# Kernel optimization log

Measured on AMD Instinct MI355X. Metric: run time of the kernel, lower is better.

## Reference

```python
import jax, jax.numpy as jnp
import numpy as np

B, T, H, P, F = 65536, 128, 1, 3, 3  # batch, input_length, hidden_dims, pred_var_dims, features


def setup_inputs() -> dict:
    key = jax.random.key(0)
    ks = jax.random.split(key, 8)
    return {
        "history_input": jax.random.normal(ks[0], (B, 1, T, F), dtype=jnp.float32),
        "h0": jnp.zeros((1, B, H), dtype=jnp.float32),
        "c0": jnp.zeros((1, B, H), dtype=jnp.float32),
        "target_acc": jax.random.normal(ks[1], (B, 1, F), dtype=jnp.float32),
        "W_ih": jax.random.normal(ks[2], (4 * H, F), dtype=jnp.float32) * 0.3,
        "W_hh": jax.random.normal(ks[3], (4 * H, H), dtype=jnp.float32) * 0.3,
        "b_ih": jnp.zeros((4 * H,), dtype=jnp.float32),
        "b_hh": jnp.zeros((4 * H,), dtype=jnp.float32),
        "W_mean": jax.random.normal(ks[4], (P, T * H), dtype=jnp.float32) * 0.05,
        "b_mean": jnp.zeros((P,), dtype=jnp.float32),
        "W_var": jax.random.normal(ks[5], (6, T * H), dtype=jnp.float32) * 0.05,
        "b_var": jnp.zeros((6,), dtype=jnp.float32),
    }


def _rotation_matrix(x):
    # x: [B, T, 3]; Gram-Schmidt on last three velocity vectors -> columns of R
    v1, v2, v3 = x[:, -1], x[:, -2], x[:, -3]
    b1 = v1 / jnp.linalg.norm(v1, axis=1, keepdims=True)
    a2 = v2 - jnp.sum(v2 * b1, axis=1, keepdims=True) * b1
    b2 = a2 / jnp.linalg.norm(a2, axis=1, keepdims=True)
    b3 = jnp.cross(b1, b2)
    sign = jnp.where(jnp.sum(v3 * b3, axis=1, keepdims=True) > 0, 1.0, -1.0)
    return jnp.stack([b1, b2, sign * b3], axis=-1)  # [B, 3, 3]


def _lstm(x, h0, c0, W_ih, W_hh, b_ih, b_hh):
    # x: [B, T, F]; PyTorch gate order i, f, g, o
    def step(carry, xt):
        h, c = carry
        g = xt @ W_ih.T + b_ih + h @ W_hh.T + b_hh
        i, f, gg, o = jnp.split(g, 4, axis=-1)
        c = jax.nn.sigmoid(f) * c + jax.nn.sigmoid(i) * jnp.tanh(gg)
        h = jax.nn.sigmoid(o) * jnp.tanh(c)
        return (h, c), h
    (hT, cT), outs = jax.lax.scan(step, (h0, c0), jnp.swapaxes(x, 0, 1))
    return jnp.swapaxes(outs, 0, 1), hT, cT  # [B, T, H]


def reference(history_input, h0, c0, target_acc, W_ih, W_hh, b_ih, b_hh,
              W_mean, b_mean, W_var, b_var):
    x = history_input[:, 0]                      # [B, T, 3]
    R = _rotation_matrix(x)                      # [B, 3, 3]
    rot = jnp.einsum('bji,bkj->bki', R, x)       # R^T @ x_k for each timestep

    out, hT, cT = _lstm(rot, h0[0], c0[0], W_ih, W_hh, b_ih, b_hh)
    feat = out.reshape(out.shape[0], -1)         # [B, T*H]
    means = feat @ W_mean.T + b_mean             # [B, 3]
    elements = feat @ W_var.T + b_var            # [B, 6]

    # unit-lower-triangular L (rows filled per cumsum index = [0, 1, 3])
    eye = jnp.eye(P, dtype=elements.dtype)
    lower = jnp.broadcast_to(eye, (elements.shape[0], P, P))
    lower = lower.at[:, 1, 0].set(elements[:, 0])
    lower = lower.at[:, 2, 0].set(elements[:, 1])
    lower = lower.at[:, 2, 1].set(elements[:, 2])
    dvals = jnp.exp(elements[:, 3:6])            # positive diagonal
    diag = dvals[:, None, :] * eye               # [B, 3, 3]
    sigma = lower @ diag @ jnp.swapaxes(lower, 1, 2)

    rot_target = jnp.einsum('bji,bj->bi', R, target_acc[:, 0])  # R^T @ a
    d = means - rot_target
    sigma_inv = jnp.linalg.inv(sigma)
    quad = jnp.einsum('bi,bij,bj->b', d, sigma_inv, d)
    logprob = -0.5 * dvals.sum(axis=1) - 0.5 * quad
    return -logprob.mean()
```

## Files before the change

kernel.cpp:

```cpp
#include <hip/hip_runtime.h>

#define T_STEPS 128
#define B_TOTAL 65536
#define BLOCK 256
#define REP 2
#define EPB (BLOCK / REP)
#define NBLOCKS (B_TOTAL / EPB)
#define CH 8
#define NCH (T_STEPS / CH)
#define R4S 7
#define FPT 3

#define LOG2E 1.44269504088896f

typedef __attribute__((ext_vector_type(2))) float f2;

__device__ __forceinline__ float fast_rcp(float x) {
    return __builtin_amdgcn_rcpf(x);
}
__device__ __forceinline__ float fast_exp2(float x) {
    return __builtin_amdgcn_exp2f(x);
}

__global__ __launch_bounds__(BLOCK, 2) void lstm_nll_main(
    const float* __restrict__ x,
    const float* __restrict__ h0,
    const float* __restrict__ c0,
    const float* __restrict__ target,
    const float* __restrict__ W_ih,
    const float* __restrict__ W_hh,
    const float* __restrict__ b_ih,
    const float* __restrict__ b_hh,
    const float* __restrict__ W_mean,
    const float* __restrict__ b_mean,
    const float* __restrict__ W_var,
    const float* __restrict__ b_var,
    float* __restrict__ partial)
{
    __shared__ __align__(16) float4 lds_x4[EPB * R4S];
    __shared__ float4 wpack4[T_STEPS * 3];
    __shared__ float  wavesum[BLOCK / 64];

    const int tid = threadIdx.x;

    for (int idx = tid; idx < T_STEPS * 3; idx += BLOCK) {
        const int t = idx / 3;
        const int k = idx - t * 3;
        float4 v;
        if (k == 0)      v = make_float4(W_mean[0*T_STEPS+t], W_mean[1*T_STEPS+t],
                                         W_mean[2*T_STEPS+t], W_var[0*T_STEPS+t]);
        else if (k == 1) v = make_float4(W_var[1*T_STEPS+t], W_var[2*T_STEPS+t],
                                         W_var[3*T_STEPS+t], W_var[4*T_STEPS+t]);
        else             v = make_float4(W_var[5*T_STEPS+t], 0.f, 0.f, 0.f);
        wpack4[idx] = v;
    }

    const int e = tid >> 1;
    const int b = blockIdx.x * EPB + e;
    const float* xb = x + (size_t)b * (T_STEPS * 3);

    const float hh0 = h0[b];
    const float cc0 = c0[b];
    const float t0 = target[b*3+0], t1 = target[b*3+1], t2 = target[b*3+2];

    const float v1x = xb[127*3+0], v1y = xb[127*3+1], v1z = xb[127*3+2];
    const float v2x = xb[126*3+0], v2y = xb[126*3+1], v2z = xb[126*3+2];
    const float v3x = xb[125*3+0], v3y = xb[125*3+1], v3z = xb[125*3+2];

    const float inv1 = rsqrtf(v1x*v1x + v1y*v1y + v1z*v1z);
    const float b1x = v1x*inv1, b1y = v1y*inv1, b1z = v1z*inv1;
    const float dp  = v2x*b1x + v2y*b1y + v2z*b1z;
    const float a2x = v2x - dp*b1x, a2y = v2y - dp*b1y, a2z = v2z - dp*b1z;
    const float inv2 = rsqrtf(a2x*a2x + a2y*a2y + a2z*a2z);
    const float b2x = a2x*inv2, b2y = a2y*inv2, b2z = a2z*inv2;
    float b3x = b1y*b2z - b1z*b2y;
    float b3y = b1z*b2x - b1x*b2z;
    float b3z = b1x*b2y - b1y*b2x;
    const float sgn = (v3x*b3x + v3y*b3y + v3z*b3z) > 0.0f ? 1.0f : -1.0f;
    b3x *= sgn; b3y *= sgn; b3z *= sgn;

    const float wi00 = W_ih[0], wi01 = W_ih[1],  wi02 = W_ih[2];
    const float wi10 = W_ih[3], wi11 = W_ih[4],  wi12 = W_ih[5];
    const float wi20 = W_ih[6], wi21 = W_ih[7],  wi22 = W_ih[8];
    const float wi30 = W_ih[9], wi31 = W_ih[10], wi32 = W_ih[11];
    const float s1 = -LOG2E, s2 = -2.0f * LOG2E;

    const f2 wAx = { s1*(wi00*b1x + wi01*b2x + wi02*b3x),
                     s1*(wi10*b1x + wi11*b2x + wi12*b3x) };
    const f2 wAy = { s1*(wi00*b1y + wi01*b2y + wi02*b3y),
                     s1*(wi10*b1y + wi11*b2y + wi12*b3y) };
    const f2 wAz = { s1*(wi00*b1z + wi01*b2z + wi02*b3z),
                     s1*(wi10*b1z + wi11*b2z + wi12*b3z) };
    const f2 wBx = { s2*(wi20*b1x + wi21*b2x + wi22*b3x),
                     s1*(wi30*b1x + wi31*b2x + wi32*b3x) };
    const f2 wBy = { s2*(wi20*b1y + wi21*b2y + wi22*b3y),
                     s1*(wi30*b1y + wi31*b2y + wi32*b3y) };
    const f2 wBz = { s2*(wi20*b1z + wi21*b2z + wi22*b3z),
                     s1*(wi30*b1z + wi31*b2z + wi32*b3z) };
    const f2 wAh = { s1*W_hh[0], s1*W_hh[1] };
    const f2 wBh = { s2*W_hh[2], s1*W_hh[3] };
    const f2 bgA = { s1*(b_ih[0] + b_hh[0]), s1*(b_ih[1] + b_hh[1]) };
    const f2 bgB = { s2*(b_ih[2] + b_hh[2]), s1*(b_ih[3] + b_hh[3]) };

    float h = hh0;
    float c = cc0;
    f2 P0 = {0.f, 0.f}, P1 = {0.f, 0.f}, P2 = {0.f, 0.f}, P3 = {0.f, 0.f};
    float e5a = 0.f;

    const float4* xg4 = (const float4*)(x + (size_t)blockIdx.x * EPB * (T_STEPS * 3));
    int ldsidx[FPT];
    int gidx[FPT];
    #pragma unroll
    for (int j = 0; j < FPT; ++j) {
        const int f = j * BLOCK + tid;
        const int r = f / 6;
        const int cc = f - r * 6;
        ldsidx[j] = r * R4S + cc;
        gidx[j]   = r * (T_STEPS * 3 / 4) + cc;
    }

    float4 pre[FPT];
    #pragma unroll
    for (int j = 0; j < FPT; ++j) pre[j] = xg4[gidx[j]];

    const float* rowp = (const float*)&lds_x4[e * R4S];

    for (int tc = 0; tc < NCH; ++tc) {
        __syncthreads();
        #pragma unroll
        for (int j = 0; j < FPT; ++j) {
            lds_x4[ldsidx[j]] = pre[j];
        }
        __syncthreads();

        f2 xdA[CH], xdB[CH];
        #pragma unroll
        for (int s = 0; s < CH; ++s) {
            const float xx = rowp[s*3+0], xy = rowp[s*3+1], xz = rowp[s*3+2];
            const f2 X = { xx, xx };
            const f2 Y = { xy, xy };
            const f2 Z = { xz, xz };
            xdA[s] = wAx*X + wAy*Y + wAz*Z + bgA;
            xdB[s] = wBx*X + wBy*Y + wBz*Z + bgB;
        }

        if (tc + 1 < NCH) {
            const int cb = (tc + 1) * 6;
            #pragma unroll
            for (int j = 0; j < FPT; ++j) pre[j] = xg4[gidx[j] + cb];
        }

        #pragma unroll
        for (int s = 0; s < CH; ++s) {
            const f2 H = { h, h };
            const f2 gA = wAh*H + xdA[s];
            const f2 gB = wBh*H + xdB[s];
            const float u = fast_exp2(gA.x);
            const float a = fast_exp2(gA.y);
            const float v = fast_exp2(gB.x);
            const float z = fast_exp2(gB.y);
            const float U = 1.0f + u, A = 1.0f + a, V = 1.0f + v;
            const float Q = U * V;
            const float num = __builtin_fmaf(c, Q, (2.0f - V) * A);
            const float den = Q * A;
            c = num * fast_rcp(den);
            const float wm = fminf(c * (-2.0f * LOG2E), 126.0f);
            const float w = fast_exp2(wm);
            const float W = 1.0f + w;
            h = (2.0f - W) * fast_rcp((1.0f + z) * W);
            const int t = tc * CH + s;
            const float4 w0 = wpack4[t*3 + 0];
            const float4 w1 = wpack4[t*3 + 1];
            const float4 w2 = wpack4[t*3 + 2];
            const f2 Hv = { h, h };
            P0 += ((f2){w0.x, w0.y}) * Hv;
            P1 += ((f2){w0.z, w0.w}) * Hv;
            P2 += ((f2){w1.x, w1.y}) * Hv;
            P3 += ((f2){w1.z, w1.w}) * Hv;
            e5a += w2.x * h;
        }
    }

    const float m0 = P0.x + b_mean[0];
    const float m1 = P0.y + b_mean[1];
    const float m2 = P1.x + b_mean[2];
    const float e0 = P1.y + b_var[0];
    const float e1 = P2.x + b_var[1];
    const float e2 = P2.y + b_var[2];
    const float e3 = P3.x + b_var[3];
    const float e4 = P3.y + b_var[4];
    const float e5 = e5a  + b_var[5];

    const float dv0 = fast_exp2(e3 * LOG2E);
    const float dv1 = fast_exp2(e4 * LOG2E);
    const float dv2 = fast_exp2(e5 * LOG2E);

    const float rt0 = b1x*t0 + b1y*t1 + b1z*t2;
    const float rt1 = b2x*t0 + b2y*t1 + b2z*t2;
    const float rt2 = b3x*t0 + b3y*t1 + b3z*t2;

    const float d0 = m0 - rt0, d1 = m1 - rt1, d2 = m2 - rt2;
    const float y0 = d0;
    const float y1 = d1 - e0 * y0;
    const float y2 = d2 - e1 * y0 - e2 * y1;
    const float quad = y0*y0*fast_rcp(dv0) + y1*y1*fast_rcp(dv1)
                     + y2*y2*fast_rcp(dv2);

    float contrib = 0.5f * (dv0 + dv1 + dv2) + 0.5f * quad;
    if ((tid & (REP - 1)) != 0) contrib = 0.0f;

    #pragma unroll
    for (int off = 32; off > 0; off >>= 1)
        contrib += __shfl_down(contrib, off, 64);
    const int lane = tid & 63, wid = tid >> 6;
    if (lane == 0) wavesum[wid] = contrib;
    __syncthreads();
    if (tid == 0) {
        float s = 0.f;
        #pragma unroll
        for (int w = 0; w < BLOCK / 64; ++w) s += wavesum[w];
        partial[blockIdx.x] = s;
    }
}

__global__ __launch_bounds__(256) void lstm_nll_finalize(
    const float* __restrict__ partial, float* __restrict__ out, int n)
{
    const int tid = threadIdx.x;
    float s = 0.0f;
    for (int i = tid; i < n; i += 256) s += partial[i];
    #pragma unroll
    for (int off = 32; off > 0; off >>= 1)
        s += __shfl_down(s, off, 64);
    __shared__ float wavesum[4];
    const int lane = tid & 63, wid = tid >> 6;
    if (lane == 0) wavesum[wid] = s;
    __syncthreads();
    if (tid == 0) {
        out[0] = (wavesum[0] + wavesum[1] + wavesum[2] + wavesum[3]) *
                 (1.0f / (float)B_TOTAL);
    }
}

extern "C" void kernel_launch(void* const* d_in, const int* in_sizes, int n_in,
                              void* d_out, int out_size, void* d_ws, size_t ws_size,
                              hipStream_t stream) {
    const float* x      = (const float*)d_in[0];
    const float* h0     = (const float*)d_in[1];
    const float* c0     = (const float*)d_in[2];
    const float* target = (const float*)d_in[3];
    const float* W_ih   = (const float*)d_in[4];
    const float* W_hh   = (const float*)d_in[5];
    const float* b_ih   = (const float*)d_in[6];
    const float* b_hh   = (const float*)d_in[7];
    const float* W_mean = (const float*)d_in[8];
    const float* b_mean = (const float*)d_in[9];
    const float* W_var  = (const float*)d_in[10];
    const float* b_var  = (const float*)d_in[11];

    float* partial = (float*)d_ws;

    lstm_nll_main<<<NBLOCKS, BLOCK, 0, stream>>>(
        x, h0, c0, target, W_ih, W_hh, b_ih, b_hh,
        W_mean, b_mean, W_var, b_var, partial);
    lstm_nll_finalize<<<1, 256, 0, stream>>>(partial, (float*)d_out, NBLOCKS);
}
```

Baseline: 193.8 us.

## Map one thread per batch element and vectorize LDS input reads

Drops the two-threads-per-element replication so each thread owns one sequence, halving block count and removing redundant LSTM arithmetic. Input chunks are read from LDS as six float4 loads per chunk, and the output projection accumulation is deferred until after the eight recurrent steps. This cuts duplicated ALU work but lowers the number of resident waves per CU, leaving less latency hiding for the serial recurrence.

```diff
diff --git a/kernel.cpp b/kernel.cpp
--- a/kernel.cpp
+++ b/kernel.cpp
@@ -3,13 +3,11 @@
 #define T_STEPS 128
 #define B_TOTAL 65536
 #define BLOCK 256
-#define REP 2
-#define EPB (BLOCK / REP)
-#define NBLOCKS (B_TOTAL / EPB)
+#define NBLOCKS (B_TOTAL / BLOCK)
 #define CH 8
 #define NCH (T_STEPS / CH)
 #define R4S 7
-#define FPT 3
+#define FPT 6
 
 #define LOG2E 1.44269504088896f
 
@@ -22,7 +20,27 @@
     return __builtin_amdgcn_exp2f(x);
 }
 
-__global__ __launch_bounds__(BLOCK, 2) void lstm_nll_main(
+__device__ __forceinline__ void lstm_step(float& h, float& c,
+                                          const f2 xdA, const f2 xdB,
+                                          const f2 wAh, const f2 wBh) {
+    const f2 H = { h, h };
+    const f2 gA = wAh * H + xdA;
+    const f2 gB = wBh * H + xdB;
+    const float u = fast_exp2(gA.x);
+    const float a = fast_exp2(gA.y);
+    const float v = fast_exp2(gB.x);
+    const float z = fast_exp2(gB.y);
+    const float U = 1.0f + u, A = 1.0f + a, V = 1.0f + v;
+    const float Q = U * V;
+    const float num = __builtin_fmaf(c, Q, (2.0f - V) * A);
+    c = num * fast_rcp(Q * A);
+    const float wm = fminf(c * (-2.0f * LOG2E), 126.0f);
+    const float w = fast_exp2(wm);
+    const float W = 1.0f + w;
+    h = (2.0f - W) * fast_rcp((1.0f + z) * W);
+}
+
+__global__ __launch_bounds__(BLOCK, 1) void lstm_nll_main(
     const float* __restrict__ x,
     const float* __restrict__ h0,
     const float* __restrict__ c0,
@@ -37,7 +55,7 @@
     const float* __restrict__ b_var,
     float* __restrict__ partial)
 {
-    __shared__ __align__(16) float4 lds_x4[EPB * R4S];
+    __shared__ __align__(16) float4 lds_x4[BLOCK * R4S];
     __shared__ float4 wpack4[T_STEPS * 3];
     __shared__ float  wavesum[BLOCK / 64];
 
@@ -55,8 +73,7 @@
         wpack4[idx] = v;
     }
 
-    const int e = tid >> 1;
-    const int b = blockIdx.x * EPB + e;
+    const int b = blockIdx.x * BLOCK + tid;
     const float* xb = x + (size_t)b * (T_STEPS * 3);
 
     const float hh0 = h0[b];
@@ -102,12 +119,31 @@
     const f2 bgA = { s1*(b_ih[0] + b_hh[0]), s1*(b_ih[1] + b_hh[1]) };
     const f2 bgB = { s2*(b_ih[2] + b_hh[2]), s1*(b_ih[3] + b_hh[3]) };
 
+    auto XA = [&](float xx, float xy, float xz) -> f2 {
+        return wAx*(f2){xx,xx} + wAy*(f2){xy,xy} + wAz*(f2){xz,xz} + bgA;
+    };
+    auto XB = [&](float xx, float xy, float xz) -> f2 {
+        return wBx*(f2){xx,xx} + wBy*(f2){xy,xy} + wBz*(f2){xz,xz} + bgB;
+    };
+
     float h = hh0;
     float c = cc0;
     f2 P0 = {0.f, 0.f}, P1 = {0.f, 0.f}, P2 = {0.f, 0.f}, P3 = {0.f, 0.f};
     float e5a = 0.f;
 
-    const float4* xg4 = (const float4*)(x + (size_t)blockIdx.x * EPB * (T_STEPS * 3));
+    auto proj = [&](int t, float hv) {
+        const float4 w0 = wpack4[t*3 + 0];
+        const float4 w1 = wpack4[t*3 + 1];
+        const float4 w2 = wpack4[t*3 + 2];
+        const f2 Hv = { hv, hv };
+        P0 += ((f2){w0.x, w0.y}) * Hv;
+        P1 += ((f2){w0.z, w0.w}) * Hv;
+        P2 += ((f2){w1.x, w1.y}) * Hv;
+        P3 += ((f2){w1.z, w1.w}) * Hv;
+        e5a += w2.x * hv;
+    };
+
+    const float4* xg4 = (const float4*)(x + (size_t)blockIdx.x * BLOCK * (T_STEPS * 3));
     int ldsidx[FPT];
     int gidx[FPT];
     #pragma unroll
@@ -123,26 +159,20 @@
     #pragma unroll
     for (int j = 0; j < FPT; ++j) pre[j] = xg4[gidx[j]];
 
-    const float* rowp = (const float*)&lds_x4[e * R4S];
+    const int rb = tid * R4S;
 
     for (int tc = 0; tc < NCH; ++tc) {
         __syncthreads();
         #pragma unroll
-        for (int j = 0; j < FPT; ++j) {
-            lds_x4[ldsidx[j]] = pre[j];
-        }
+        for (int j = 0; j < FPT; ++j) lds_x4[ldsidx[j]] = pre[j];
         __syncthreads();
 
-        f2 xdA[CH], xdB[CH];
-        #pragma unroll
-        for (int s = 0; s < CH; ++s) {
-            const float xx = rowp[s*3+0], xy = rowp[s*3+1], xz = rowp[s*3+2];
-            const f2 X = { xx, xx };
-            const f2 Y = { xy, xy };
-            const f2 Z = { xz, xz };
-            xdA[s] = wAx*X + wAy*Y + wAz*Z + bgA;
-            xdB[s] = wBx*X + wBy*Y + wBz*Z + bgB;
-        }
+        const float4 q0 = lds_x4[rb + 0];
+        const float4 q1 = lds_x4[rb + 1];
+        const float4 q2 = lds_x4[rb + 2];
+        const float4 q3 = lds_x4[rb + 3];
+        const float4 q4 = lds_x4[rb + 4];
+        const float4 q5 = lds_x4[rb + 5];
 
         if (tc + 1 < NCH) {
             const int cb = (tc + 1) * 6;
@@ -150,35 +180,33 @@
             for (int j = 0; j < FPT; ++j) pre[j] = xg4[gidx[j] + cb];
         }
 
-        #pragma unroll
-        for (int s = 0; s < CH; ++s) {
-            const f2 H = { h, h };
-            const f2 gA = wAh*H + xdA[s];
-            const f2 gB = wBh*H + xdB[s];
-            const float u = fast_exp2(gA.x);
-            const float a = fast_exp2(gA.y);
-            const float v = fast_exp2(gB.x);
-            const float z = fast_exp2(gB.y);
-            const float U = 1.0f + u, A = 1.0f + a, V = 1.0f + v;
-            const float Q = U * V;
-            const float num = __builtin_fmaf(c, Q, (2.0f - V) * A);
-            const float den = Q * A;
-            c = num * fast_rcp(den);
-            const float wm = fminf(c * (-2.0f * LOG2E), 126.0f);
-            const float w = fast_exp2(wm);
-            const float W = 1.0f + w;
-            h = (2.0f - W) * fast_rcp((1.0f + z) * W);
-            const int t = tc * CH + s;
-            const float4 w0 = wpack4[t*3 + 0];
-            const float4 w1 = wpack4[t*3 + 1];
-            const float4 w2 = wpack4[t*3 + 2];
-            const f2 Hv = { h, h };
-            P0 += ((f2){w0.x, w0.y}) * Hv;
-            P1 += ((f2){w0.z, w0.w}) * Hv;
-            P2 += ((f2){w1.x, w1.y}) * Hv;
-            P3 += ((f2){w1.z, w1.w}) * Hv;
-            e5a += w2.x * h;
-        }
+        const f2 dA0 = XA(q0.x, q0.y, q0.z), dB0 = XB(q0.x, q0.y, q0.z);
+        const f2 dA1 = XA(q0.w, q1.x, q1.y), dB1 = XB(q0.w, q1.x, q1.y);
+        const f2 dA2 = XA(q1.z, q1.w, q2.x), dB2 = XB(q1.z, q1.w, q2.x);
+        const f2 dA3 = XA(q2.y, q2.z, q2.w), dB3 = XB(q2.y, q2.z, q2.w);
+        const f2 dA4 = XA(q3.x, q3.y, q3.z), dB4 = XB(q3.x, q3.y, q3.z);
+        const f2 dA5 = XA(q3.w, q4.x, q4.y), dB5 = XB(q3.w, q4.x, q4.y);
+        const f2 dA6 = XA(q4.z, q4.w, q5.x), dB6 = XB(q4.z, q4.w, q5.x);
+        const f2 dA7 = XA(q5.y, q5.z, q5.w), dB7 = XB(q5.y, q5.z, q5.w);
+
+        lstm_step(h, c, dA0, dB0, wAh, wBh); const float hv0 = h;
+        lstm_step(h, c, dA1, dB1, wAh, wBh); const float hv1 = h;
+        lstm_step(h, c, dA2, dB2, wAh, wBh); const float hv2 = h;
+        lstm_step(h, c, dA3, dB3, wAh, wBh); const float hv3 = h;
+        lstm_step(h, c, dA4, dB4, wAh, wBh); const float hv4 = h;
+        lstm_step(h, c, dA5, dB5, wAh, wBh); const float hv5 = h;
+        lstm_step(h, c, dA6, dB6, wAh, wBh); const float hv6 = h;
+        lstm_step(h, c, dA7, dB7, wAh, wBh); const float hv7 = h;
+
+        const int tb = tc * CH;
+        proj(tb + 0, hv0);
+        proj(tb + 1, hv1);
+        proj(tb + 2, hv2);
+        proj(tb + 3, hv3);
+        proj(tb + 4, hv4);
+        proj(tb + 5, hv5);
+        proj(tb + 6, hv6);
+        proj(tb + 7, hv7);
     }
 
     const float m0 = P0.x + b_mean[0];
@@ -207,7 +235,6 @@
                      + y2*y2*fast_rcp(dv2);
 
     float contrib = 0.5f * (dv0 + dv1 + dv2) + 0.5f * quad;
-    if ((tid & (REP - 1)) != 0) contrib = 0.0f;
 
     #pragma unroll
     for (int off = 32; off > 0; off >>= 1)
```

Measured after the change: 228.4 us. +17.8%, slower.
